# Performance work log

Measured on AMD Instinct MI355X. Metric: run time of the kernel, lower is better.

Reference implementation:

```python
import jax, jax.numpy as jnp
import numpy as np

B, S, D = 2, 2048, 2048
HQ, HKV, HD, HDV = 32, 8, 64, 64
QPK = HQ // HKV
EPS = 1e-5


def setup_inputs() -> dict:
    key = jax.random.key(0)
    ks = jax.random.split(key, 10)
    s = lambda fan_in: 1.0 / np.sqrt(fan_in)
    return {
        'x': jax.random.normal(ks[0], (B, S, D), dtype=jnp.float32),
        'ln_g': jnp.ones((D,), jnp.float32),
        'ln_b': jnp.zeros((D,), jnp.float32),
        'Wq': jax.random.uniform(ks[1], (D, HQ * HD), jnp.float32, -s(D), s(D)),
        'bq': jax.random.uniform(ks[2], (HQ * HD,), jnp.float32, -s(D), s(D)),
        'Wk': jax.random.uniform(ks[3], (D, HKV * HD), jnp.float32, -s(D), s(D)),
        'bk': jax.random.uniform(ks[4], (HKV * HD,), jnp.float32, -s(D), s(D)),
        'Wv': jax.random.uniform(ks[5], (D, HKV * HDV), jnp.float32, -s(D), s(D)),
        'bv': jax.random.uniform(ks[6], (HKV * HDV,), jnp.float32, -s(D), s(D)),
        'Wo': jax.random.uniform(ks[7], (HQ * HDV, D), jnp.float32, -s(HQ * HDV), s(HQ * HDV)),
        'bo': jax.random.uniform(ks[8], (D,), jnp.float32, -s(HQ * HDV), s(HQ * HDV)),
    }


def reference(x, ln_g, ln_b, Wq, bq, Wk, bk, Wv, bv, Wo, bo):
    # LayerNorm
    mu = jnp.mean(x, axis=-1, keepdims=True)
    var = jnp.mean(jnp.square(x - mu), axis=-1, keepdims=True)
    xn = (x - mu) * jax.lax.rsqrt(var + EPS) * ln_g + ln_b

    q = (xn @ Wq + bq).reshape(B, S, HKV, QPK, HD) * (1.0 / np.sqrt(HD))
    k = (xn @ Wk + bk).reshape(B, S, HKV, HD)
    v = (xn @ Wv + bv).reshape(B, S, HKV, HDV)

    # scores: (b, t=query, T=key, h, q_per_kv)
    scores = jnp.einsum('bthqd,bThd->btThq', q, k)
    # causal mask: -inf where T > t (upper triangle above diagonal)
    mask = jnp.triu(jnp.full((S, S), -jnp.inf, dtype=scores.dtype), 1)
    scores = scores + mask[None, :, :, None, None]
    # NOTE: source softmaxes over dim=-4, i.e. the QUERY axis t -> axis=1 here
    scores = jax.nn.softmax(scores, axis=1)
    out = jnp.einsum('btThq,bThd->bthqd', scores, v)
    out = out.reshape(B, S, HQ * HDV)
    return out @ Wo + bo
```

## Files before the change

### kernel.cpp

```cpp
#include <hip/hip_runtime.h>

#define Bb  2
#define Ss  2048
#define Dd  2048
#define HKV 8
#define QPK 4
#define HD  64
#define MR  (Bb * Ss)
#define NQ  2048
#define NKV 512

#define LOG2E 1.4426950408889634f

typedef unsigned short u16;
typedef unsigned int u32;
typedef __attribute__((ext_vector_type(8))) short s16x8;
typedef __attribute__((ext_vector_type(4))) float f32x4;

__device__ __forceinline__ u16 f2bf(float f) {
  unsigned u = __float_as_uint(f);
  u += 0x7fffu + ((u >> 16) & 1u);
  return (u16)(u >> 16);
}

__device__ __forceinline__ void gload16(const u16* g, u16* l) {
  __builtin_amdgcn_global_load_lds(
      (const __attribute__((address_space(1))) unsigned int*)g,
      (__attribute__((address_space(3))) unsigned int*)l, 16, 0, 0);
}

__device__ __forceinline__ u32 cvtpk_bf16(float a, float b) {
  u32 r;
  asm volatile("v_cvt_pk_bf16_f32 %0, %1, %2" : "=v"(r) : "v"(a), "v"(b));
  return r;
}

#define BAR()    asm volatile("s_barrier" ::: "memory")
#define WAITV4() asm volatile("s_waitcnt vmcnt(4)" ::: "memory")
#define WAITV0() asm volatile("s_waitcnt vmcnt(0)" ::: "memory")

__global__ __launch_bounds__(256) void ln_kernel(
    const float* __restrict__ x, const float* __restrict__ g,
    const float* __restrict__ be, u16* __restrict__ xn)
{
  int row = blockIdx.x;
  int tid = threadIdx.x;
  const float4* xr = (const float4*)(x + (size_t)row * Dd);
  float4 a = xr[tid];
  float4 b4 = xr[tid + 256];
  float s  = a.x + a.y + a.z + a.w + b4.x + b4.y + b4.z + b4.w;
  float ss = a.x*a.x + a.y*a.y + a.z*a.z + a.w*a.w
           + b4.x*b4.x + b4.y*b4.y + b4.z*b4.z + b4.w*b4.w;
  #pragma unroll
  for (int off = 32; off > 0; off >>= 1) {
    s  += __shfl_down(s, off);
    ss += __shfl_down(ss, off);
  }
  __shared__ float red[8];
  int lane = tid & 63, w = tid >> 6;
  if (lane == 0) { red[w] = s; red[4 + w] = ss; }
  __syncthreads();
  s  = red[0] + red[1] + red[2] + red[3];
  ss = red[4] + red[5] + red[6] + red[7];
  float mu = s * (1.0f / Dd);
  float rs = rsqrtf(ss * (1.0f / Dd) - mu * mu + 1e-5f);

  u16* xo = xn + (size_t)row * Dd;
  const float4* gv4 = (const float4*)g;
  const float4* bv4 = (const float4*)be;
  #pragma unroll
  for (int p = 0; p < 2; ++p) {
    int idx = tid + p * 256;
    float4 xv = (p == 0) ? a : b4;
    float4 gg = gv4[idx], bb = bv4[idx];
    ushort4 pk;
    pk.x = f2bf((xv.x - mu) * rs * gg.x + bb.x);
    pk.y = f2bf((xv.y - mu) * rs * gg.y + bb.y);
    pk.z = f2bf((xv.z - mu) * rs * gg.z + bb.z);
    pk.w = f2bf((xv.w - mu) * rs * gg.w + bb.w);
    *(ushort4*)(xo + idx * 4) = pk;
  }
}

__global__ __launch_bounds__(256) void transpose_cast(
    const float* __restrict__ W, u16* __restrict__ WT, int K, int N)
{
  __shared__ float tile[32][33];
  int tx = threadIdx.x & 31, ty = threadIdx.x >> 5;
  int n0 = blockIdx.x * 32, k0 = blockIdx.y * 32;
  #pragma unroll
  for (int i = 0; i < 4; ++i)
    tile[ty + 8 * i][tx] = W[(size_t)(k0 + ty + 8 * i) * N + n0 + tx];
  __syncthreads();
  #pragma unroll
  for (int i = 0; i < 4; ++i)
    WT[(size_t)(n0 + ty + 8 * i) * K + k0 + tx] = f2bf(tile[tx][ty + 8 * i]);
}

__global__ __launch_bounds__(256) void transpose_v(
    const u16* __restrict__ vb, u16* __restrict__ vT)
{
  __shared__ u16 tile[32][33];
  int tx = threadIdx.x & 31, ty = threadIdx.x >> 5;
  int c0 = blockIdx.x * 32;
  int r0 = blockIdx.y * 32;
  #pragma unroll
  for (int i = 0; i < 4; ++i)
    tile[ty + 8 * i][tx] = vb[(size_t)(r0 + ty + 8 * i) * NKV + c0 + tx];
  __syncthreads();
  int b = r0 >> 11, t = r0 & 2047;
  #pragma unroll
  for (int i = 0; i < 4; ++i)
    vT[((size_t)(b * NKV + c0 + ty + 8 * i)) * Ss + t + tx] = tile[tx][ty + 8 * i];
}

__device__ __forceinline__ void gemm8_core(
    const u16* __restrict__ A, const u16* __restrict__ BT, int K,
    int brow, int bcol, u16* __restrict__ As, u16* __restrict__ Bs,
    f32x4 (&acc)[8][4])
{
  const int tid  = threadIdx.x;
  const int lane = tid & 63;
  const int wave = tid >> 6;
  const int wr = wave >> 2, wc = wave & 3;
  const int m16 = lane & 15, quad = lane >> 4;
  const int NT = K >> 6;

  const int r0 = tid >> 3;
  const int sg = (tid & 7) ^ (r0 & 7);
  const u16* Asrc = A  + (size_t)(brow + r0) * K + sg * 8;
  const u16* Bsrc = BT + (size_t)(bcol + r0) * K + sg * 8;
  u16* AsW = As + wave * 512;
  u16* BsW = Bs + wave * 512;
  const size_t a64 = (size_t)64 * K;

  const int sl0 = (quad ^ (m16 & 7)) * 8;
  const int sl1 = ((quad | 4) ^ (m16 & 7)) * 8;
  const u16* Afr = As + wr * 8192 + m16 * 64;
  const u16* Bfr = Bs + (wc >> 1) * 8192 + ((wc & 1) * 64 + m16) * 64;

  #pragma unroll
  for (int h = 0; h < 2; ++h) {
    gload16(Asrc + (size_t)(h * 128) * K, AsW + h * 8192);
    gload16(Asrc + (size_t)(h * 128) * K + a64, AsW + h * 8192 + 4096);
    gload16(Bsrc + (size_t)(h * 128) * K, BsW + h * 8192);
    gload16(Bsrc + (size_t)(h * 128) * K + a64, BsW + h * 8192 + 4096);
  }
  #pragma unroll
  for (int h = 0; h < 2; ++h) {
    gload16(Bsrc + (size_t)(h * 128) * K + 64, BsW + 16384 + h * 8192);
    gload16(Bsrc + (size_t)(h * 128) * K + a64 + 64, BsW + 16384 + h * 8192 + 4096);
  }
  WAITV4();
  BAR();

  for (int t = 0; t < NT; ++t) {
    const int bi = t & 1;
    const u16* Abuf = Afr + bi * 16384;
    const u16* Bbuf = Bfr + bi * 16384;
    s16x8 bfr[4][2];
    #pragma unroll
    for (int ph = 0; ph < 4; ++ph) {
      s16x8 a0k0 = *(const s16x8*)(Abuf + (ph * 2 + 0) * 1024 + sl0);
      s16x8 a0k1 = *(const s16x8*)(Abuf + (ph * 2 + 0) * 1024 + sl1);
      s16x8 a1k0 = *(const s16x8*)(Abuf + (ph * 2 + 1) * 1024 + sl0);
      s16x8 a1k1 = *(const s16x8*)(Abuf + (ph * 2 + 1) * 1024 + sl1);
      if (ph == 0) {
        #pragma unroll
        for (int nj = 0; nj < 4; ++nj) {
          bfr[nj][0] = *(const s16x8*)(Bbuf + nj * 1024 + sl0);
          bfr[nj][1] = *(const s16x8*)(Bbuf + nj * 1024 + sl1);
        }
      }
      if (ph < 2) {
        if (t + 1 < NT) {
          const u16* g = Asrc + (size_t)(ph * 128) * K + (t + 1) * 64;
          u16* l = AsW + (bi ^ 1) * 16384 + ph * 8192;
          gload16(g, l);
          gload16(g + a64, l + 4096);
        }
      } else {
        if (t + 2 < NT) {
          const u16* g = Bsrc + (size_t)((ph - 2) * 128) * K + (t + 2) * 64;
          u16* l = BsW + bi * 16384 + (ph - 2) * 8192;
          gload16(g, l);
          gload16(g + a64, l + 4096);
        }
      }
      BAR();
      __builtin_amdgcn_s_setprio(1);
      #pragma unroll
      for (int nj = 0; nj < 4; ++nj) {
        acc[ph*2+0][nj] = __builtin_amdgcn_mfma_f32_16x16x32_bf16(a0k0, bfr[nj][0], acc[ph*2+0][nj], 0, 0, 0);
        acc[ph*2+0][nj] = __builtin_amdgcn_mfma_f32_16x16x32_bf16(a0k1, bfr[nj][1], acc[ph*2+0][nj], 0, 0, 0);
        acc[ph*2+1][nj] = __builtin_amdgcn_mfma_f32_16x16x32_bf16(a1k0, bfr[nj][0], acc[ph*2+1][nj], 0, 0, 0);
        acc[ph*2+1][nj] = __builtin_amdgcn_mfma_f32_16x16x32_bf16(a1k1, bfr[nj][1], acc[ph*2+1][nj], 0, 0, 0);
      }
      __builtin_amdgcn_s_setprio(0);
      if (ph == 3) {
        if (t + 2 < NT) WAITV4(); else WAITV0();
      }
      BAR();
    }
  }
}

__global__ __launch_bounds__(512) void gemm8_bt(
    const u16* __restrict__ A, const u16* __restrict__ BT,
    const float* __restrict__ bias, float* __restrict__ C, int N, int K)
{
  __shared__ u16 As[32768];
  __shared__ u16 Bs[32768];
  int nbx = N >> 8;
  int id  = blockIdx.y * nbx + blockIdx.x;
  int nwg = gridDim.x * gridDim.y;
  int swz = (id & 7) * (nwg >> 3) + (id >> 3);
  int bx = swz % nbx, by = swz / nbx;

  f32x4 acc[8][4] = {};
  gemm8_core(A, BT, K, by * 256, bx * 256, As, Bs, acc);

  int lane = threadIdx.x & 63, wave = threadIdx.x >> 6;
  int wr = wave >> 2, wc = wave & 3;
  int m16 = lane & 15, quad = lane >> 4;
  int colb = bx * 256 + (wc >> 1) * 128 + (wc & 1) * 64;
  #pragma unroll
  for (int nj = 0; nj < 4; ++nj) {
    int col = colb + nj * 16 + m16;
    float bc = bias[col];
    #pragma unroll
    for (int mi = 0; mi < 8; ++mi)
      #pragma unroll
      for (int rr = 0; rr < 4; ++rr) {
        int row = by * 256 + wr * 128 + mi * 16 + quad * 4 + rr;
        C[(size_t)row * N + col] = acc[mi][nj][rr] + bc;
      }
  }
}

__global__ __launch_bounds__(512) void gemm8_qkv(
    const u16* __restrict__ A, const u16* __restrict__ BT,
    const float* __restrict__ bq, const float* __restrict__ bk,
    const float* __restrict__ bv,
    u16* __restrict__ qb, u16* __restrict__ kb, u16* __restrict__ vb)
{
  __shared__ u16 As[32768];
  __shared__ u16 Bs[32768];
  int nbx = 12;
  int id  = blockIdx.y * nbx + blockIdx.x;
  int nwg = 192;
  int swz = (id & 7) * (nwg >> 3) + (id >> 3);
  int bx = swz % nbx, by = swz / nbx;

  f32x4 acc[8][4] = {};
  gemm8_core(A, BT, Dd, by * 256, bx * 256, As, Bs, acc);

  u16* outp; const float* bp; int ldo, cb; float scale;
  if (bx < 8)       { outp = qb; bp = bq; ldo = NQ;  cb = bx * 256;        scale = 0.125f * LOG2E; }
  else if (bx < 10) { outp = kb; bp = bk; ldo = NKV; cb = (bx - 8) * 256;  scale = 1.0f; }
  else              { outp = vb; bp = bv; ldo = NKV; cb = (bx - 10) * 256; scale = 1.0f; }

  int lane = threadIdx.x & 63, wave = threadIdx.x >> 6;
  int wr = wave >> 2, wc = wave & 3;
  int m16 = lane & 15, quad = lane >> 4;
  int colb = cb + (wc >> 1) * 128 + (wc & 1) * 64;
  #pragma unroll
  for (int nj = 0; nj < 4; ++nj) {
    int col = colb + nj * 16 + m16;
    float bc = bp[col];
    #pragma unroll
    for (int mi = 0; mi < 8; ++mi)
      #pragma unroll
      for (int rr = 0; rr < 4; ++rr) {
        int row = by * 256 + wr * 128 + mi * 16 + quad * 4 + rr;
        outp[(size_t)row * ldo + col] = f2bf((acc[mi][nj][rr] + bc) * scale);
      }
  }
}

__global__ __launch_bounds__(256) void pass_a_mfma(
    const u16* __restrict__ qb, const u16* __restrict__ kb,
    float* __restrict__ cst)
{
  __shared__ u16 Qs[64 * 64];
  int combo = blockIdx.x;
  int qk = combo & 3, bh = combo >> 2;
  int b = bh >> 3, h = bh & 7;
  int g = blockIdx.y;
  int tid = threadIdx.x;
  int lane = tid & 63, wave = tid >> 6;
  int m16 = lane & 15, quad = lane >> 4;
  int T0w = g * 128 + wave * 32;

  const u16* kbase = kb + (size_t)b * Ss * NKV + h * HD;
  const u16* qbase = qb + (size_t)b * Ss * NQ + (h * QPK + qk) * HD;

  s16x8 kf[2][2];
  #pragma unroll
  for (int jg = 0; jg < 2; ++jg)
    #pragma unroll
    for (int dc = 0; dc < 2; ++dc)
      kf[jg][dc] = *(const s16x8*)(kbase + (size_t)(T0w + jg * 16 + m16) * NKV + dc * 32 + quad * 8);

  float ms[2] = {-1e30f, -1e30f};
  float ls[2] = {0.f, 0.f};
  int srow  = (wave << 3) + (lane >> 3);
  int slot0 = (lane & 7) ^ (lane >> 3);
  u16* QsW = Qs + (size_t)(wave * 8) * 64;
  int sl0 = quad ^ (m16 & 7);
  int sl1 = (quad | 4) ^ (m16 & 7);
  int tDiag = T0w & ~63;

  for (int t0 = g * 128; t0 < Ss; t0 += 64) {
    __syncthreads();
    gload16(qbase + (size_t)(t0 + srow) * NQ + slot0 * 8, QsW);
    gload16(qbase + (size_t)(t0 + srow + 32) * NQ + slot0 * 8, QsW + 32 * 64);
    __syncthreads();
    if (t0 + 63 < T0w) continue;

    s16x8 af[4][2];
    #pragma unroll
    for (int i = 0; i < 4; ++i) {
      af[i][0] = *(const s16x8*)&Qs[(i * 16 + m16) * 64 + sl0 * 8];
      af[i][1] = *(const s16x8*)&Qs[(i * 16 + m16) * 64 + sl1 * 8];
    }
    f32x4 acc[4][2];
    #pragma unroll
    for (int i = 0; i < 4; ++i)
      #pragma unroll
      for (int jg = 0; jg < 2; ++jg) {
        f32x4 z = {};
        z = __builtin_amdgcn_mfma_f32_16x16x32_bf16(af[i][0], kf[jg][0], z, 0, 0, 0);
        acc[i][jg] = __builtin_amdgcn_mfma_f32_16x16x32_bf16(af[i][1], kf[jg][1], z, 0, 0, 0);
      }
    if (t0 == tDiag) {
      #pragma unroll
      for (int i = 0; i < 4; ++i)
        #pragma unroll
        for (int jg = 0; jg < 2; ++jg) {
          int tg = t0 + i * 16 + quad * 4;
          int Tg = T0w + jg * 16 + m16;
          #pragma unroll
          for (int r = 0; r < 4; ++r)
            if (tg + r < Tg) acc[i][jg][r] = -3e38f;
        }
    }
    #pragma unroll
    for (int jg = 0; jg < 2; ++jg) {
      float bm = -3e38f;
      #pragma unroll
      for (int i = 0; i < 4; ++i)
        #pragma unroll
        for (int r = 0; r < 4; ++r) bm = fmaxf(bm, acc[i][jg][r]);
      float mn = fmaxf(ms[jg], bm);
      float se = 0.f;
      #pragma unroll
      for (int i = 0; i < 4; ++i)
        #pragma unroll
        for (int r = 0; r < 4; ++r) se += exp2f(acc[i][jg][r] - mn);
      ls[jg] = ls[jg] * exp2f(ms[jg] - mn) + se;
      ms[jg] = mn;
    }
  }
  #pragma unroll
  for (int jg = 0; jg < 2; ++jg) {
    float m = ms[jg], l = ls[jg];
    #pragma unroll
    for (int off = 16; off <= 32; off <<= 1) {
      float mo = __shfl_xor(m, off);
      float lo = __shfl_xor(l, off);
      float mn = fmaxf(m, mo);
      l = l * exp2f(m - mn) + lo * exp2f(mo - mn);
      m = mn;
    }
    if (quad == 0)
      cst[(size_t)(bh * QPK + qk) * Ss + T0w + jg * 16 + m16] = m + __log2f(l);
  }
}

__global__ __launch_bounds__(256) void pass_b_mfma(
    const u16* __restrict__ qb, const u16* __restrict__ kb,
    const u16* __restrict__ vT, const float* __restrict__ cst,
    u16* __restrict__ attn)
{
  __shared__ u16 Ks[64 * 64];
  __shared__ u16 Vs[64 * 64];
  int combo = blockIdx.x;
  int qk = combo & 3, bh = combo >> 2;
  int b = bh >> 3, h = bh & 7;
  int g = 31 - blockIdx.y;
  int tid = threadIdx.x;
  int lane = tid & 63, wave = tid >> 6;
  int m16 = lane & 15, quad = lane >> 4;
  int trow = g * 64 + wave * 16;

  const u16* qbase = qb + (size_t)b * Ss * NQ + (h * QPK + qk) * HD;
  const u16* kbase = kb + (size_t)b * Ss * NKV + h * HD;
  const u16* vbase = vT + (size_t)(bh * 64) * Ss;
  const float* cbase = cst + (size_t)(bh * QPK + qk) * Ss;

  s16x8 qf[2];
  #pragma unroll
  for (int dc = 0; dc < 2; ++dc)
    qf[dc] = *(const s16x8*)(qbase + (size_t)(trow + m16) * NQ + dc * 32 + quad * 8);

  f32x4 oacc[4] = {};
  int srow  = (wave << 3) + (lane >> 3);
  int slot0 = (lane & 7) ^ (lane >> 3);
  u16* KsW = Ks + (size_t)(wave * 8) * 64;
  u16* VsW = Vs + (size_t)(wave * 8) * 64;
  int sl0 = quad ^ (m16 & 7);
  int sl1 = (quad | 4) ^ (m16 & 7);
  int Tend = g * 64;

  for (int T0 = 0; T0 <= Tend; T0 += 64) {
    __syncthreads();
    gload16(kbase + (size_t)(T0 + srow) * NKV + slot0 * 8, KsW);
    gload16(kbase + (size_t)(T0 + srow + 32) * NKV + slot0 * 8, KsW + 32 * 64);
    gload16(vbase + (size_t)srow * Ss + T0 + slot0 * 8, VsW);
    gload16(vbase + (size_t)(srow + 32) * Ss + T0 + slot0 * 8, VsW + 32 * 64);
    __syncthreads();
    bool diag = (T0 == Tend);
    #pragma unroll
    for (int tc = 0; tc < 2; ++tc) {
      u32 A[2], Bw[2];
      #pragma unroll
      for (int ii = 0; ii < 2; ++ii) {
        int i = tc * 2 + ii;
        s16x8 k0 = *(const s16x8*)&Ks[(i * 16 + m16) * 64 + sl0 * 8];
        s16x8 k1 = *(const s16x8*)&Ks[(i * 16 + m16) * 64 + sl1 * 8];
        f32x4 z = {};
        z = __builtin_amdgcn_mfma_f32_16x16x32_bf16(k0, qf[0], z, 0, 0, 0);
        z = __builtin_amdgcn_mfma_f32_16x16x32_bf16(k1, qf[1], z, 0, 0, 0);
        float4 cc = *(const float4*)(cbase + T0 + i * 16 + quad * 4);
        float w0 = exp2f(z[0] - cc.x);
        float w1 = exp2f(z[1] - cc.y);
        float w2 = exp2f(z[2] - cc.z);
        float w3 = exp2f(z[3] - cc.w);
        if (diag) {
          int t  = trow + m16;
          int Tg = T0 + i * 16 + quad * 4;
          if (Tg + 0 > t) w0 = 0.f;
          if (Tg + 1 > t) w1 = 0.f;
          if (Tg + 2 > t) w2 = 0.f;
          if (Tg + 3 > t) w3 = 0.f;
        }
        A[ii]  = cvtpk_bf16(w0, w1);
        Bw[ii] = cvtpk_bf16(w2, w3);
      }
      asm volatile("v_permlane32_swap_b32 %0, %1" : "+v"(A[0]),  "+v"(A[1]));
      asm volatile("v_permlane16_swap_b32 %0, %1" : "+v"(A[0]),  "+v"(A[1]));
      asm volatile("v_permlane32_swap_b32 %0, %1" : "+v"(Bw[0]), "+v"(Bw[1]));
      asm volatile("v_permlane16_swap_b32 %0, %1" : "+v"(Bw[0]), "+v"(Bw[1]));
      union { uint4 u; s16x8 v; } pu;
      pu.u.x = A[0]; pu.u.y = Bw[0]; pu.u.z = A[1]; pu.u.w = Bw[1];
      s16x8 pa = pu.v;
      #pragma unroll
      for (int dj = 0; dj < 4; ++dj) {
        int vsl = (quad | (tc << 2)) ^ (m16 & 7);
        s16x8 vf = *(const s16x8*)&Vs[(dj * 16 + m16) * 64 + vsl * 8];
        oacc[dj] = __builtin_amdgcn_mfma_f32_16x16x32_bf16(pa, vf, oacc[dj], 0, 0, 0);
      }
    }
  }
  u16* abase = attn + (size_t)b * Ss * NQ + (h * QPK + qk) * HD;
  #pragma unroll
  for (int dj = 0; dj < 4; ++dj)
    #pragma unroll
    for (int r = 0; r < 4; ++r)
      abase[(size_t)(trow + quad * 4 + r) * NQ + dj * 16 + m16] = f2bf(oacc[dj][r]);
}

extern "C" void kernel_launch(void* const* d_in, const int* in_sizes, int n_in,
                              void* d_out, int out_size, void* d_ws, size_t ws_size,
                              hipStream_t stream)
{
  (void)in_sizes; (void)n_in; (void)out_size; (void)ws_size;
  const float* x   = (const float*)d_in[0];
  const float* lng = (const float*)d_in[1];
  const float* lnb = (const float*)d_in[2];
  const float* Wq  = (const float*)d_in[3];
  const float* bq  = (const float*)d_in[4];
  const float* Wk  = (const float*)d_in[5];
  const float* bk  = (const float*)d_in[6];
  const float* Wv  = (const float*)d_in[7];
  const float* bv  = (const float*)d_in[8];
  const float* Wo  = (const float*)d_in[9];
  const float* bo  = (const float*)d_in[10];
  float* out = (float*)d_out;

  char* ws = (char*)d_ws;
  size_t off = 0;
  auto take = [&](size_t bytes) -> char* {
    char* p = ws + off;
    off += (bytes + 255) & ~(size_t)255;
    return p;
  };
  u16*    xnb   = (u16*)take((size_t)MR * Dd * 2);
  u16*    wqkvT = (u16*)take((size_t)(NQ + 2 * NKV) * Dd * 2);
  u16*    woT   = (u16*)take((size_t)Dd * NQ * 2);
  u16*    qbB   = (u16*)take((size_t)MR * NQ * 2);
  u16*    kbB   = (u16*)take((size_t)MR * NKV * 2);
  u16*    vbB   = (u16*)take((size_t)MR * NKV * 2);
  u16*    vTb   = (u16*)take((size_t)MR * NKV * 2);
  float*  cst   = (float*)take((size_t)Bb * HKV * QPK * Ss * 4);
  u16*    attnb = (u16*)take((size_t)MR * NQ * 2);

  ln_kernel<<<MR, 256, 0, stream>>>(x, lng, lnb, xnb);
  transpose_cast<<<dim3(NQ / 32, Dd / 32), 256, 0, stream>>>(Wq, wqkvT, Dd, NQ);
  transpose_cast<<<dim3(NKV / 32, Dd / 32), 256, 0, stream>>>(Wk, wqkvT + (size_t)NQ * Dd, Dd, NKV);
  transpose_cast<<<dim3(NKV / 32, Dd / 32), 256, 0, stream>>>(Wv, wqkvT + (size_t)(NQ + NKV) * Dd, Dd, NKV);
  transpose_cast<<<dim3(NQ / 32, Dd / 32), 256, 0, stream>>>(Wo, woT, Dd, NQ);

  gemm8_qkv<<<dim3(12, 16), 512, 0, stream>>>(xnb, wqkvT, bq, bk, bv, qbB, kbB, vbB);
  transpose_v<<<dim3(NKV / 32, MR / 32), 256, 0, stream>>>(vbB, vTb);

  pass_a_mfma<<<dim3(64, 16), 256, 0, stream>>>(qbB, kbB, cst);
  pass_b_mfma<<<dim3(64, 32), 256, 0, stream>>>(qbB, kbB, vTb, cst, attnb);

  gemm8_bt<<<dim3(8, 16), 512, 0, stream>>>(attnb, woT, bo, out, Dd, NQ);
}
```

Measured before the change: 385.6 us.

## Pair causal tiles for balanced attention blocks and use narrower output GEMM tiles

```diff
diff --git a/kernel.cpp b/kernel.cpp
--- a/kernel.cpp
+++ b/kernel.cpp
@@ -37,6 +37,7 @@
 
 #define BAR()    asm volatile("s_barrier" ::: "memory")
 #define WAITV4() asm volatile("s_waitcnt vmcnt(4)" ::: "memory")
+#define WAITV2() asm volatile("s_waitcnt vmcnt(2)" ::: "memory")
 #define WAITV0() asm volatile("s_waitcnt vmcnt(0)" ::: "memory")
 
 __global__ __launch_bounds__(256) void ln_kernel(
@@ -205,39 +206,6 @@
   }
 }
 
-__global__ __launch_bounds__(512) void gemm8_bt(
-    const u16* __restrict__ A, const u16* __restrict__ BT,
-    const float* __restrict__ bias, float* __restrict__ C, int N, int K)
-{
-  __shared__ u16 As[32768];
-  __shared__ u16 Bs[32768];
-  int nbx = N >> 8;
-  int id  = blockIdx.y * nbx + blockIdx.x;
-  int nwg = gridDim.x * gridDim.y;
-  int swz = (id & 7) * (nwg >> 3) + (id >> 3);
-  int bx = swz % nbx, by = swz / nbx;
-
-  f32x4 acc[8][4] = {};
-  gemm8_core(A, BT, K, by * 256, bx * 256, As, Bs, acc);
-
-  int lane = threadIdx.x & 63, wave = threadIdx.x >> 6;
-  int wr = wave >> 2, wc = wave & 3;
-  int m16 = lane & 15, quad = lane >> 4;
-  int colb = bx * 256 + (wc >> 1) * 128 + (wc & 1) * 64;
-  #pragma unroll
-  for (int nj = 0; nj < 4; ++nj) {
-    int col = colb + nj * 16 + m16;
-    float bc = bias[col];
-    #pragma unroll
-    for (int mi = 0; mi < 8; ++mi)
-      #pragma unroll
-      for (int rr = 0; rr < 4; ++rr) {
-        int row = by * 256 + wr * 128 + mi * 16 + quad * 4 + rr;
-        C[(size_t)row * N + col] = acc[mi][nj][rr] + bc;
-      }
-  }
-}
-
 __global__ __launch_bounds__(512) void gemm8_qkv(
     const u16* __restrict__ A, const u16* __restrict__ BT,
     const float* __restrict__ bq, const float* __restrict__ bk,
@@ -278,6 +246,117 @@
   }
 }
 
+__global__ __launch_bounds__(512) void gemm8_wo(
+    const u16* __restrict__ A, const u16* __restrict__ BT,
+    const float* __restrict__ bias, float* __restrict__ C, int N, int K)
+{
+  __shared__ u16 As[32768];
+  __shared__ u16 Bs[16384];
+  int nbx = N >> 7;
+  int id  = blockIdx.y * nbx + blockIdx.x;
+  int nwg = gridDim.x * gridDim.y;
+  int swz = (id & 7) * (nwg >> 3) + (id >> 3);
+  int bx = swz % nbx, by = swz / nbx;
+
+  const int tid  = threadIdx.x;
+  const int lane = tid & 63;
+  const int wave = tid >> 6;
+  const int wr = wave >> 2, wc = wave & 3;
+  const int m16 = lane & 15, quad = lane >> 4;
+  const int NT = K >> 6;
+
+  const int r0 = tid >> 3;
+  const int sg = (tid & 7) ^ (r0 & 7);
+  const u16* Asrc = A  + (size_t)(by * 256 + r0) * K + sg * 8;
+  const u16* Bsrc = BT + (size_t)(bx * 128 + r0) * K + sg * 8;
+  u16* AsW = As + wave * 512;
+  u16* BsW = Bs + wave * 512;
+  const size_t a64 = (size_t)64 * K;
+
+  const int sl0 = (quad ^ (m16 & 7)) * 8;
+  const int sl1 = ((quad | 4) ^ (m16 & 7)) * 8;
+  const u16* Afr = As + wr * 8192 + m16 * 64;
+  const u16* Bfr = Bs + (wc * 32 + m16) * 64;
+
+  f32x4 acc[8][2] = {};
+
+  #pragma unroll
+  for (int h = 0; h < 2; ++h) {
+    gload16(Asrc + (size_t)(h * 128) * K, AsW + h * 8192);
+    gload16(Asrc + (size_t)(h * 128) * K + a64, AsW + h * 8192 + 4096);
+  }
+  gload16(Bsrc, BsW);
+  gload16(Bsrc + a64, BsW + 4096);
+  gload16(Bsrc + 64, BsW + 8192);
+  gload16(Bsrc + a64 + 64, BsW + 8192 + 4096);
+  WAITV2();
+  BAR();
+
+  for (int t = 0; t < NT; ++t) {
+    const int bi = t & 1;
+    const u16* Abuf = Afr + bi * 16384;
+    const u16* Bbuf = Bfr + bi * 8192;
+    s16x8 bfr[2][2];
+    #pragma unroll
+    for (int ph = 0; ph < 4; ++ph) {
+      s16x8 a0k0 = *(const s16x8*)(Abuf + (ph * 2 + 0) * 1024 + sl0);
+      s16x8 a0k1 = *(const s16x8*)(Abuf + (ph * 2 + 0) * 1024 + sl1);
+      s16x8 a1k0 = *(const s16x8*)(Abuf + (ph * 2 + 1) * 1024 + sl0);
+      s16x8 a1k1 = *(const s16x8*)(Abuf + (ph * 2 + 1) * 1024 + sl1);
+      if (ph == 0) {
+        #pragma unroll
+        for (int nj = 0; nj < 2; ++nj) {
+          bfr[nj][0] = *(const s16x8*)(Bbuf + nj * 1024 + sl0);
+          bfr[nj][1] = *(const s16x8*)(Bbuf + nj * 1024 + sl1);
+        }
+      }
+      if (ph < 2) {
+        if (t + 1 < NT) {
+          const u16* g = Asrc + (size_t)(ph * 128) * K + (t + 1) * 64;
+          u16* l = AsW + (bi ^ 1) * 16384 + ph * 8192;
+          gload16(g, l);
+          gload16(g + a64, l + 4096);
+        }
+      } else if (ph == 2) {
+        if (t + 2 < NT) {
+          const u16* g = Bsrc + (size_t)(t + 2) * 64;
+          u16* l = BsW + bi * 8192;
+          gload16(g, l);
+          gload16(g + a64, l + 4096);
+        }
+      }
+      BAR();
+      __builtin_amdgcn_s_setprio(1);
+      #pragma unroll
+      for (int nj = 0; nj < 2; ++nj) {
+        acc[ph*2+0][nj] = __builtin_amdgcn_mfma_f32_16x16x32_bf16(a0k0, bfr[nj][0], acc[ph*2+0][nj], 0, 0, 0);
+        acc[ph*2+0][nj] = __builtin_amdgcn_mfma_f32_16x16x32_bf16(a0k1, bfr[nj][1], acc[ph*2+0][nj], 0, 0, 0);
+        acc[ph*2+1][nj] = __builtin_amdgcn_mfma_f32_16x16x32_bf16(a1k0, bfr[nj][0], acc[ph*2+1][nj], 0, 0, 0);
+        acc[ph*2+1][nj] = __builtin_amdgcn_mfma_f32_16x16x32_bf16(a1k1, bfr[nj][1], acc[ph*2+1][nj], 0, 0, 0);
+      }
+      __builtin_amdgcn_s_setprio(0);
+      if (ph == 3) {
+        if (t + 2 < NT) WAITV2(); else WAITV0();
+      }
+      BAR();
+    }
+  }
+
+  int colb = bx * 128 + wc * 32;
+  #pragma unroll
+  for (int nj = 0; nj < 2; ++nj) {
+    int col = colb + nj * 16 + m16;
+    float bc = bias[col];
+    #pragma unroll
+    for (int mi = 0; mi < 8; ++mi)
+      #pragma unroll
+      for (int rr = 0; rr < 4; ++rr) {
+        int row = by * 256 + wr * 128 + mi * 16 + quad * 4 + rr;
+        C[(size_t)row * N + col] = acc[mi][nj][rr] + bc;
+      }
+  }
+}
+
 __global__ __launch_bounds__(256) void pass_a_mfma(
     const u16* __restrict__ qb, const u16* __restrict__ kb,
     float* __restrict__ cst)
@@ -286,37 +365,42 @@
   int combo = blockIdx.x;
   int qk = combo & 3, bh = combo >> 2;
   int b = bh >> 3, h = bh & 7;
-  int g = blockIdx.y;
+  int gi = blockIdx.y;
+  int gA = gi, gB = 15 - gi;
   int tid = threadIdx.x;
   int lane = tid & 63, wave = tid >> 6;
   int m16 = lane & 15, quad = lane >> 4;
-  int T0w = g * 128 + wave * 32;
+  int T0wA = gA * 128 + wave * 32;
+  int T0wB = gB * 128 + wave * 32;
 
   const u16* kbase = kb + (size_t)b * Ss * NKV + h * HD;
   const u16* qbase = qb + (size_t)b * Ss * NQ + (h * QPK + qk) * HD;
 
-  s16x8 kf[2][2];
+  s16x8 kfA[2][2], kfB[2][2];
   #pragma unroll
   for (int jg = 0; jg < 2; ++jg)
     #pragma unroll
-    for (int dc = 0; dc < 2; ++dc)
-      kf[jg][dc] = *(const s16x8*)(kbase + (size_t)(T0w + jg * 16 + m16) * NKV + dc * 32 + quad * 8);
-
-  float ms[2] = {-1e30f, -1e30f};
-  float ls[2] = {0.f, 0.f};
+    for (int dc = 0; dc < 2; ++dc) {
+      kfA[jg][dc] = *(const s16x8*)(kbase + (size_t)(T0wA + jg * 16 + m16) * NKV + dc * 32 + quad * 8);
+      kfB[jg][dc] = *(const s16x8*)(kbase + (size_t)(T0wB + jg * 16 + m16) * NKV + dc * 32 + quad * 8);
+    }
+
+  float msA[2] = {-1e30f, -1e30f}, lsA[2] = {0.f, 0.f};
+  float msB[2] = {-1e30f, -1e30f}, lsB[2] = {0.f, 0.f};
   int srow  = (wave << 3) + (lane >> 3);
   int slot0 = (lane & 7) ^ (lane >> 3);
   u16* QsW = Qs + (size_t)(wave * 8) * 64;
   int sl0 = quad ^ (m16 & 7);
   int sl1 = (quad | 4) ^ (m16 & 7);
-  int tDiag = T0w & ~63;
-
-  for (int t0 = g * 128; t0 < Ss; t0 += 64) {
+  int tDiagA = T0wA & ~63;
+  int tDiagB = T0wB & ~63;
+
+  for (int t0 = gA * 128; t0 < Ss; t0 += 64) {
     __syncthreads();
     gload16(qbase + (size_t)(t0 + srow) * NQ + slot0 * 8, QsW);
     gload16(qbase + (size_t)(t0 + srow + 32) * NQ + slot0 * 8, QsW + 32 * 64);
     __syncthreads();
-    if (t0 + 63 < T0w) continue;
+    if (t0 + 63 < T0wA) continue;
 
     s16x8 af[4][2];
     #pragma unroll
@@ -324,47 +408,88 @@
       af[i][0] = *(const s16x8*)&Qs[(i * 16 + m16) * 64 + sl0 * 8];
       af[i][1] = *(const s16x8*)&Qs[(i * 16 + m16) * 64 + sl1 * 8];
     }
-    f32x4 acc[4][2];
-    #pragma unroll
-    for (int i = 0; i < 4; ++i)
+    {
+      f32x4 acc[4][2];
+      #pragma unroll
+      for (int i = 0; i < 4; ++i)
+        #pragma unroll
+        for (int jg = 0; jg < 2; ++jg) {
+          f32x4 z = {};
+          z = __builtin_amdgcn_mfma_f32_16x16x32_bf16(af[i][0], kfA[jg][0], z, 0, 0, 0);
+          acc[i][jg] = __builtin_amdgcn_mfma_f32_16x16x32_bf16(af[i][1], kfA[jg][1], z, 0, 0, 0);
+        }
+      if (t0 == tDiagA) {
+        #pragma unroll
+        for (int i = 0; i < 4; ++i)
+          #pragma unroll
+          for (int jg = 0; jg < 2; ++jg) {
+            int tg = t0 + i * 16 + quad * 4;
+            int Tg = T0wA + jg * 16 + m16;
+            #pragma unroll
+            for (int r = 0; r < 4; ++r)
+              if (tg + r < Tg) acc[i][jg][r] = -3e38f;
+          }
+      }
       #pragma unroll
       for (int jg = 0; jg < 2; ++jg) {
-        f32x4 z = {};
-        z = __builtin_amdgcn_mfma_f32_16x16x32_bf16(af[i][0], kf[jg][0], z, 0, 0, 0);
-        acc[i][jg] = __builtin_amdgcn_mfma_f32_16x16x32_bf16(af[i][1], kf[jg][1], z, 0, 0, 0);
-      }
-    if (t0 == tDiag) {
+        float bm = -3e38f;
+        #pragma unroll
+        for (int i = 0; i < 4; ++i)
+          #pragma unroll
+          for (int r = 0; r < 4; ++r) bm = fmaxf(bm, acc[i][jg][r]);
+        float mn = fmaxf(msA[jg], bm);
+        float se = 0.f;
+        #pragma unroll
+        for (int i = 0; i < 4; ++i)
+          #pragma unroll
+          for (int r = 0; r < 4; ++r) se += exp2f(acc[i][jg][r] - mn);
+        lsA[jg] = lsA[jg] * exp2f(msA[jg] - mn) + se;
+        msA[jg] = mn;
+      }
+    }
+    if (t0 + 63 >= T0wB) {
+      f32x4 acc[4][2];
       #pragma unroll
       for (int i = 0; i < 4; ++i)
         #pragma unroll
         for (int jg = 0; jg < 2; ++jg) {
-          int tg = t0 + i * 16 + quad * 4;
-          int Tg = T0w + jg * 16 + m16;
+          f32x4 z = {};
+          z = __builtin_amdgcn_mfma_f32_16x16x32_bf16(af[i][0], kfB[jg][0], z, 0, 0, 0);
+          acc[i][jg] = __builtin_amdgcn_mfma_f32_16x16x32_bf16(af[i][1], kfB[jg][1], z, 0, 0, 0);
+        }
+      if (t0 == tDiagB) {
+        #pragma unroll
+        for (int i = 0; i < 4; ++i)
           #pragma unroll
-          for (int r = 0; r < 4; ++r)
-            if (tg + r < Tg) acc[i][jg][r] = -3e38f;
-        }
-    }
-    #pragma unroll
-    for (int jg = 0; jg < 2; ++jg) {
-      float bm = -3e38f;
-      #pragma unroll
-      for (int i = 0; i < 4; ++i)
-        #pragma unroll
-        for (int r = 0; r < 4; ++r) bm = fmaxf(bm, acc[i][jg][r]);
-      float mn = fmaxf(ms[jg], bm);
-      float se = 0.f;
-      #pragma unroll
-      for (int i = 0; i < 4; ++i)
-        #pragma unroll
-        for (int r = 0; r < 4; ++r) se += exp2f(acc[i][jg][r] - mn);
-      ls[jg] = ls[jg] * exp2f(ms[jg] - mn) + se;
-      ms[jg] = mn;
+          for (int jg = 0; jg < 2; ++jg) {
+            int tg = t0 + i * 16 + quad * 4;
+            int Tg = T0wB + jg * 16 + m16;
+            #pragma unroll
+            for (int r = 0; r < 4; ++r)
+              if (tg + r < Tg) acc[i][jg][r] = -3e38f;
+          }
+      }
+      #pragma unroll
+      for (int jg = 0; jg < 2; ++jg) {
+        float bm = -3e38f;
+        #pragma unroll
+        for (int i = 0; i < 4; ++i)
+          #pragma unroll
+          for (int r = 0; r < 4; ++r) bm = fmaxf(bm, acc[i][jg][r]);
+        float mn = fmaxf(msB[jg], bm);
+        float se = 0.f;
+        #pragma unroll
+        for (int i = 0; i < 4; ++i)
+          #pragma unroll
+          for (int r = 0; r < 4; ++r) se += exp2f(acc[i][jg][r] - mn);
+        lsB[jg] = lsB[jg] * exp2f(msB[jg] - mn) + se;
+        msB[jg] = mn;
+      }
     }
   }
   #pragma unroll
   for (int jg = 0; jg < 2; ++jg) {
-    float m = ms[jg], l = ls[jg];
+    float m = msA[jg], l = lsA[jg];
     #pragma unroll
     for (int off = 16; off <= 32; off <<= 1) {
       float mo = __shfl_xor(m, off);
@@ -374,7 +499,21 @@
       m = mn;
     }
     if (quad == 0)
-      cst[(size_t)(bh * QPK + qk) * Ss + T0w + jg * 16 + m16] = m + __log2f(l);
+      cst[(size_t)(bh * QPK + qk) * Ss + T0wA + jg * 16 + m16] = m + __log2f(l);
+  }
+  #pragma unroll
+  for (int jg = 0; jg < 2; ++jg) {
+    float m = msB[jg], l = lsB[jg];
+    #pragma unroll
+    for (int off = 16; off <= 32; off <<= 1) {
+      float mo = __shfl_xor(m, off);
+      float lo = __shfl_xor(l, off);
+      float mn = fmaxf(m, mo);
+      l = l * exp2f(m - mn) + lo * exp2f(mo - mn);
+      m = mn;
+    }
+    if (quad == 0)
+      cst[(size_t)(bh * QPK + qk) * Ss + T0wB + jg * 16 + m16] = m + __log2f(l);
   }
 }
 
@@ -388,78 +527,121 @@
   int combo = blockIdx.x;
   int qk = combo & 3, bh = combo >> 2;
   int b = bh >> 3, h = bh & 7;
-  int g = 31 - blockIdx.y;
+  int gi = blockIdx.y;
   int tid = threadIdx.x;
   int lane = tid & 63, wave = tid >> 6;
   int m16 = lane & 15, quad = lane >> 4;
-  int trow = g * 64 + wave * 16;
+  int trowH = (31 - gi) * 64 + wave * 16;
+  int trowL = gi * 64 + wave * 16;
+  int TendH = (31 - gi) * 64;
+  int TendL = gi * 64;
 
   const u16* qbase = qb + (size_t)b * Ss * NQ + (h * QPK + qk) * HD;
   const u16* kbase = kb + (size_t)b * Ss * NKV + h * HD;
   const u16* vbase = vT + (size_t)(bh * 64) * Ss;
   const float* cbase = cst + (size_t)(bh * QPK + qk) * Ss;
 
-  s16x8 qf[2];
-  #pragma unroll
-  for (int dc = 0; dc < 2; ++dc)
-    qf[dc] = *(const s16x8*)(qbase + (size_t)(trow + m16) * NQ + dc * 32 + quad * 8);
-
-  f32x4 oacc[4] = {};
+  s16x8 qfH[2], qfL[2];
+  #pragma unroll
+  for (int dc = 0; dc < 2; ++dc) {
+    qfH[dc] = *(const s16x8*)(qbase + (size_t)(trowH + m16) * NQ + dc * 32 + quad * 8);
+    qfL[dc] = *(const s16x8*)(qbase + (size_t)(trowL + m16) * NQ + dc * 32 + quad * 8);
+  }
+
+  f32x4 oaccH[4] = {}, oaccL[4] = {};
   int srow  = (wave << 3) + (lane >> 3);
   int slot0 = (lane & 7) ^ (lane >> 3);
   u16* KsW = Ks + (size_t)(wave * 8) * 64;
   u16* VsW = Vs + (size_t)(wave * 8) * 64;
   int sl0 = quad ^ (m16 & 7);
   int sl1 = (quad | 4) ^ (m16 & 7);
-  int Tend = g * 64;
-
-  for (int T0 = 0; T0 <= Tend; T0 += 64) {
+
+  for (int T0 = 0; T0 <= TendH; T0 += 64) {
     __syncthreads();
     gload16(kbase + (size_t)(T0 + srow) * NKV + slot0 * 8, KsW);
     gload16(kbase + (size_t)(T0 + srow + 32) * NKV + slot0 * 8, KsW + 32 * 64);
     gload16(vbase + (size_t)srow * Ss + T0 + slot0 * 8, VsW);
     gload16(vbase + (size_t)(srow + 32) * Ss + T0 + slot0 * 8, VsW + 32 * 64);
     __syncthreads();
-    bool diag = (T0 == Tend);
+    bool doL   = (T0 <= TendL);
+    bool diagH = (T0 == TendH);
+    bool diagL = (T0 == TendL);
     #pragma unroll
     for (int tc = 0; tc < 2; ++tc) {
-      u32 A[2], Bw[2];
+      u32 AH[2], BH[2], AL[2], BL[2];
       #pragma unroll
       for (int ii = 0; ii < 2; ++ii) {
         int i = tc * 2 + ii;
         s16x8 k0 = *(const s16x8*)&Ks[(i * 16 + m16) * 64 + sl0 * 8];
         s16x8 k1 = *(const s16x8*)&Ks[(i * 16 + m16) * 64 + sl1 * 8];
-        f32x4 z = {};
-        z = __builtin_amdgcn_mfma_f32_16x16x32_bf16(k0, qf[0], z, 0, 0, 0);
-        z = __builtin_amdgcn_mfma_f32_16x16x32_bf16(k1, qf[1], z, 0, 0, 0);
         float4 cc = *(const float4*)(cbase + T0 + i * 16 + quad * 4);
-        float w0 = exp2f(z[0] - cc.x);
-        float w1 = exp2f(z[1] - cc.y);
-        float w2 = exp2f(z[2] - cc.z);
-        float w3 = exp2f(z[3] - cc.w);
-        if (diag) {
-          int t  = trow + m16;
-          int Tg = T0 + i * 16 + quad * 4;
-          if (Tg + 0 > t) w0 = 0.f;
-          if (Tg + 1 > t) w1 = 0.f;
-          if (Tg + 2 > t) w2 = 0.f;
-          if (Tg + 3 > t) w3 = 0.f;
-        }
-        A[ii]  = cvtpk_bf16(w0, w1);
-        Bw[ii] = cvtpk_bf16(w2, w3);
-      }
-      asm volatile("v_permlane32_swap_b32 %0, %1" : "+v"(A[0]),  "+v"(A[1]));
-      asm volatile("v_permlane16_swap_b32 %0, %1" : "+v"(A[0]),  "+v"(A[1]));
-      asm volatile("v_permlane32_swap_b32 %0, %1" : "+v"(Bw[0]), "+v"(Bw[1]));
-      asm volatile("v_permlane16_swap_b32 %0, %1" : "+v"(Bw[0]), "+v"(Bw[1]));
-      union { uint4 u; s16x8 v; } pu;
-      pu.u.x = A[0]; pu.u.y = Bw[0]; pu.u.z = A[1]; pu.u.w = Bw[1];
-      s16x8 pa = pu.v;
-      #pragma unroll
-      for (int dj = 0; dj < 4; ++dj) {
-        int vsl = (quad | (tc << 2)) ^ (m16 & 7);
-        s16x8 vf = *(const s16x8*)&Vs[(dj * 16 + m16) * 64 + vsl * 8];
-        oacc[dj] = __builtin_amdgcn_mfma_f32_16x16x32_bf16(pa, vf, oacc[dj], 0, 0, 0);
+        int Tg = T0 + i * 16 + quad * 4;
+        {
+          f32x4 z = {};
+          z = __builtin_amdgcn_mfma_f32_16x16x32_bf16(k0, qfH[0], z, 0, 0, 0);
+          z = __builtin_amdgcn_mfma_f32_16x16x32_bf16(k1, qfH[1], z, 0, 0, 0);
+          float w0 = exp2f(z[0] - cc.x);
+          float w1 = exp2f(z[1] - cc.y);
+          float w2 = exp2f(z[2] - cc.z);
+          float w3 = exp2f(z[3] - cc.w);
+          if (diagH) {
+            int t = trowH + m16;
+            if (Tg + 0 > t) w0 = 0.f;
+            if (Tg + 1 > t) w1 = 0.f;
+            if (Tg + 2 > t) w2 = 0.f;
+            if (Tg + 3 > t) w3 = 0.f;
+          }
+          AH[ii] = cvtpk_bf16(w0, w1);
+          BH[ii] = cvtpk_bf16(w2, w3);
+        }
+        if (doL) {
+          f32x4 z = {};
+          z = __builtin_amdgcn_mfma_f32_16x16x32_bf16(k0, qfL[0], z, 0, 0, 0);
+          z = __builtin_amdgcn_mfma_f32_16x16x32_bf16(k1, qfL[1], z, 0, 0, 0);
+          float w0 = exp2f(z[0] - cc.x);
+          float w1 = exp2f(z[1] - cc.y);
+          float w2 = exp2f(z[2] - cc.z);
+          float w3 = exp2f(z[3] - cc.w);
+          if (diagL) {
+            int t = trowL + m16;
+            if (Tg + 0 > t) w0 = 0.f;
+            if (Tg + 1 > t) w1 = 0.f;
+            if (Tg + 2 > t) w2 = 0.f;
+            if (Tg + 3 > t) w3 = 0.f;
+          }
+          AL[ii] = cvtpk_bf16(w0, w1);
+          BL[ii] = cvtpk_bf16(w2, w3);
+        }
+      }
+      asm volatile("v_permlane32_swap_b32 %0, %1" : "+v"(AH[0]), "+v"(AH[1]));
+      asm volatile("v_permlane16_swap_b32 %0, %1" : "+v"(AH[0]), "+v"(AH[1]));
+      asm volatile("v_permlane32_swap_b32 %0, %1" : "+v"(BH[0]), "+v"(BH[1]));
+      asm volatile("v_permlane16_swap_b32 %0, %1" : "+v"(BH[0]), "+v"(BH[1]));
+      {
+        union { uint4 u; s16x8 v; } pu;
+        pu.u.x = AH[0]; pu.u.y = BH[0]; pu.u.z = AH[1]; pu.u.w = BH[1];
+        s16x8 pa = pu.v;
+        #pragma unroll
+        for (int dj = 0; dj < 4; ++dj) {
+          int vsl = (quad | (tc << 2)) ^ (m16 & 7);
+          s16x8 vf = *(const s16x8*)&Vs[(dj * 16 + m16) * 64 + vsl * 8];
+          oaccH[dj] = __builtin_amdgcn_mfma_f32_16x16x32_bf16(pa, vf, oaccH[dj], 0, 0, 0);
+        }
+      }
+      if (doL) {
+        asm volatile("v_permlane32_swap_b32 %0, %1" : "+v"(AL[0]), "+v"(AL[1]));
+        asm volatile("v_permlane16_swap_b32 %0, %1" : "+v"(AL[0]), "+v"(AL[1]));
+        asm volatile("v_permlane32_swap_b32 %0, %1" : "+v"(BL[0]), "+v"(BL[1]));
+        asm volatile("v_permlane16_swap_b32 %0, %1" : "+v"(BL[0]), "+v"(BL[1]));
+        union { uint4 u; s16x8 v; } pu;
+        pu.u.x = AL[0]; pu.u.y = BL[0]; pu.u.z = AL[1]; pu.u.w = BL[1];
+        s16x8 pa = pu.v;
+        #pragma unroll
+        for (int dj = 0; dj < 4; ++dj) {
+          int vsl = (quad | (tc << 2)) ^ (m16 & 7);
+          s16x8 vf = *(const s16x8*)&Vs[(dj * 16 + m16) * 64 + vsl * 8];
+          oaccL[dj] = __builtin_amdgcn_mfma_f32_16x16x32_bf16(pa, vf, oaccL[dj], 0, 0, 0);
+        }
       }
     }
   }
@@ -467,8 +649,10 @@
   #pragma unroll
   for (int dj = 0; dj < 4; ++dj)
     #pragma unroll
-    for (int r = 0; r < 4; ++r)
-      abase[(size_t)(trow + quad * 4 + r) * NQ + dj * 16 + m16] = f2bf(oacc[dj][r]);
+    for (int r = 0; r < 4; ++r) {
+      abase[(size_t)(trowH + quad * 4 + r) * NQ + dj * 16 + m16] = f2bf(oaccH[dj][r]);
+      abase[(size_t)(trowL + quad * 4 + r) * NQ + dj * 16 + m16] = f2bf(oaccL[dj][r]);
+    }
 }
 
 extern "C" void kernel_launch(void* const* d_in, const int* in_sizes, int n_in,
@@ -515,8 +699,8 @@
   gemm8_qkv<<<dim3(12, 16), 512, 0, stream>>>(xnb, wqkvT, bq, bk, bv, qbB, kbB, vbB);
   transpose_v<<<dim3(NKV / 32, MR / 32), 256, 0, stream>>>(vbB, vTb);
 
-  pass_a_mfma<<<dim3(64, 16), 256, 0, stream>>>(qbB, kbB, cst);
-  pass_b_mfma<<<dim3(64, 32), 256, 0, stream>>>(qbB, kbB, vTb, cst, attnb);
-
-  gemm8_bt<<<dim3(8, 16), 512, 0, stream>>>(attnb, woT, bo, out, Dd, NQ);
-}
+  pass_a_mfma<<<dim3(64, 8), 256, 0, stream>>>(qbB, kbB, cst);
+  pass_b_mfma<<<dim3(64, 16), 256, 0, stream>>>(qbB, kbB, vTb, cst, attnb);
+
+  gemm8_wo<<<dim3(16, 16), 512, 0, stream>>>(attnb, woT, bo, out, Dd, NQ);
+}
```

Result: slower. 430.1 us (+11.5%).

## Double-buffer Q/K tiles in attention passes and use 256x128 output GEMM tiles

Applied to the files above, without the earlier changes.

```diff
diff --git a/kernel.cpp b/kernel.cpp
--- a/kernel.cpp
+++ b/kernel.cpp
@@ -37,6 +37,7 @@
 
 #define BAR()    asm volatile("s_barrier" ::: "memory")
 #define WAITV4() asm volatile("s_waitcnt vmcnt(4)" ::: "memory")
+#define WAITV2() asm volatile("s_waitcnt vmcnt(2)" ::: "memory")
 #define WAITV0() asm volatile("s_waitcnt vmcnt(0)" ::: "memory")
 
 __global__ __launch_bounds__(256) void ln_kernel(
@@ -205,39 +206,6 @@
   }
 }
 
-__global__ __launch_bounds__(512) void gemm8_bt(
-    const u16* __restrict__ A, const u16* __restrict__ BT,
-    const float* __restrict__ bias, float* __restrict__ C, int N, int K)
-{
-  __shared__ u16 As[32768];
-  __shared__ u16 Bs[32768];
-  int nbx = N >> 8;
-  int id  = blockIdx.y * nbx + blockIdx.x;
-  int nwg = gridDim.x * gridDim.y;
-  int swz = (id & 7) * (nwg >> 3) + (id >> 3);
-  int bx = swz % nbx, by = swz / nbx;
-
-  f32x4 acc[8][4] = {};
-  gemm8_core(A, BT, K, by * 256, bx * 256, As, Bs, acc);
-
-  int lane = threadIdx.x & 63, wave = threadIdx.x >> 6;
-  int wr = wave >> 2, wc = wave & 3;
-  int m16 = lane & 15, quad = lane >> 4;
-  int colb = bx * 256 + (wc >> 1) * 128 + (wc & 1) * 64;
-  #pragma unroll
-  for (int nj = 0; nj < 4; ++nj) {
-    int col = colb + nj * 16 + m16;
-    float bc = bias[col];
-    #pragma unroll
-    for (int mi = 0; mi < 8; ++mi)
-      #pragma unroll
-      for (int rr = 0; rr < 4; ++rr) {
-        int row = by * 256 + wr * 128 + mi * 16 + quad * 4 + rr;
-        C[(size_t)row * N + col] = acc[mi][nj][rr] + bc;
-      }
-  }
-}
-
 __global__ __launch_bounds__(512) void gemm8_qkv(
     const u16* __restrict__ A, const u16* __restrict__ BT,
     const float* __restrict__ bq, const float* __restrict__ bk,
@@ -278,11 +246,122 @@
   }
 }
 
+__global__ __launch_bounds__(512) void gemm8_wo(
+    const u16* __restrict__ A, const u16* __restrict__ BT,
+    const float* __restrict__ bias, float* __restrict__ C, int N, int K)
+{
+  __shared__ u16 As[32768];
+  __shared__ u16 Bs[16384];
+  int nbx = N >> 7;
+  int id  = blockIdx.y * nbx + blockIdx.x;
+  int nwg = gridDim.x * gridDim.y;
+  int swz = (id & 7) * (nwg >> 3) + (id >> 3);
+  int bx = swz % nbx, by = swz / nbx;
+
+  const int tid  = threadIdx.x;
+  const int lane = tid & 63;
+  const int wave = tid >> 6;
+  const int wr = wave >> 2, wc = wave & 3;
+  const int m16 = lane & 15, quad = lane >> 4;
+  const int NT = K >> 6;
+
+  const int r0 = tid >> 3;
+  const int sg = (tid & 7) ^ (r0 & 7);
+  const u16* Asrc = A  + (size_t)(by * 256 + r0) * K + sg * 8;
+  const u16* Bsrc = BT + (size_t)(bx * 128 + r0) * K + sg * 8;
+  u16* AsW = As + wave * 512;
+  u16* BsW = Bs + wave * 512;
+  const size_t a64 = (size_t)64 * K;
+
+  const int sl0 = (quad ^ (m16 & 7)) * 8;
+  const int sl1 = ((quad | 4) ^ (m16 & 7)) * 8;
+  const u16* Afr = As + wr * 8192 + m16 * 64;
+  const u16* Bfr = Bs + (wc * 32 + m16) * 64;
+
+  f32x4 acc[8][2] = {};
+
+  #pragma unroll
+  for (int h = 0; h < 2; ++h) {
+    gload16(Asrc + (size_t)(h * 128) * K, AsW + h * 8192);
+    gload16(Asrc + (size_t)(h * 128) * K + a64, AsW + h * 8192 + 4096);
+  }
+  gload16(Bsrc, BsW);
+  gload16(Bsrc + a64, BsW + 4096);
+  gload16(Bsrc + 64, BsW + 8192);
+  gload16(Bsrc + a64 + 64, BsW + 8192 + 4096);
+  WAITV2();
+  BAR();
+
+  for (int t = 0; t < NT; ++t) {
+    const int bi = t & 1;
+    const u16* Abuf = Afr + bi * 16384;
+    const u16* Bbuf = Bfr + bi * 8192;
+    s16x8 bfr[2][2];
+    #pragma unroll
+    for (int ph = 0; ph < 4; ++ph) {
+      s16x8 a0k0 = *(const s16x8*)(Abuf + (ph * 2 + 0) * 1024 + sl0);
+      s16x8 a0k1 = *(const s16x8*)(Abuf + (ph * 2 + 0) * 1024 + sl1);
+      s16x8 a1k0 = *(const s16x8*)(Abuf + (ph * 2 + 1) * 1024 + sl0);
+      s16x8 a1k1 = *(const s16x8*)(Abuf + (ph * 2 + 1) * 1024 + sl1);
+      if (ph == 0) {
+        #pragma unroll
+        for (int nj = 0; nj < 2; ++nj) {
+          bfr[nj][0] = *(const s16x8*)(Bbuf + nj * 1024 + sl0);
+          bfr[nj][1] = *(const s16x8*)(Bbuf + nj * 1024 + sl1);
+        }
+      }
+      if (ph < 2) {
+        if (t + 1 < NT) {
+          const u16* g = Asrc + (size_t)(ph * 128) * K + (t + 1) * 64;
+          u16* l = AsW + (bi ^ 1) * 16384 + ph * 8192;
+          gload16(g, l);
+          gload16(g + a64, l + 4096);
+        }
+      } else if (ph == 2) {
+        if (t + 2 < NT) {
+          const u16* g = Bsrc + (size_t)(t + 2) * 64;
+          u16* l = BsW + bi * 8192;
+          gload16(g, l);
+          gload16(g + a64, l + 4096);
+        }
+      }
+      BAR();
+      __builtin_amdgcn_s_setprio(1);
+      #pragma unroll
+      for (int nj = 0; nj < 2; ++nj) {
+        acc[ph*2+0][nj] = __builtin_amdgcn_mfma_f32_16x16x32_bf16(a0k0, bfr[nj][0], acc[ph*2+0][nj], 0, 0, 0);
+        acc[ph*2+0][nj] = __builtin_amdgcn_mfma_f32_16x16x32_bf16(a0k1, bfr[nj][1], acc[ph*2+0][nj], 0, 0, 0);
+        acc[ph*2+1][nj] = __builtin_amdgcn_mfma_f32_16x16x32_bf16(a1k0, bfr[nj][0], acc[ph*2+1][nj], 0, 0, 0);
+        acc[ph*2+1][nj] = __builtin_amdgcn_mfma_f32_16x16x32_bf16(a1k1, bfr[nj][1], acc[ph*2+1][nj], 0, 0, 0);
+      }
+      __builtin_amdgcn_s_setprio(0);
+      if (ph == 3) {
+        if (t + 2 < NT) WAITV2(); else WAITV0();
+      }
+      BAR();
+    }
+  }
+
+  int colb = bx * 128 + wc * 32;
+  #pragma unroll
+  for (int nj = 0; nj < 2; ++nj) {
+    int col = colb + nj * 16 + m16;
+    float bc = bias[col];
+    #pragma unroll
+    for (int mi = 0; mi < 8; ++mi)
+      #pragma unroll
+      for (int rr = 0; rr < 4; ++rr) {
+        int row = by * 256 + wr * 128 + mi * 16 + quad * 4 + rr;
+        C[(size_t)row * N + col] = acc[mi][nj][rr] + bc;
+      }
+  }
+}
+
 __global__ __launch_bounds__(256) void pass_a_mfma(
     const u16* __restrict__ qb, const u16* __restrict__ kb,
     float* __restrict__ cst)
 {
-  __shared__ u16 Qs[64 * 64];
+  __shared__ u16 Qs[2][64 * 64];
   int combo = blockIdx.x;
   int qk = combo & 3, bh = combo >> 2;
   int b = bh >> 3, h = bh & 7;
@@ -306,23 +385,37 @@
   float ls[2] = {0.f, 0.f};
   int srow  = (wave << 3) + (lane >> 3);
   int slot0 = (lane & 7) ^ (lane >> 3);
-  u16* QsW = Qs + (size_t)(wave * 8) * 64;
   int sl0 = quad ^ (m16 & 7);
   int sl1 = (quad | 4) ^ (m16 & 7);
   int tDiag = T0w & ~63;
 
-  for (int t0 = g * 128; t0 < Ss; t0 += 64) {
-    __syncthreads();
+  {
+    u16* QsW = &Qs[0][(wave * 8) * 64];
+    int t0 = g * 128;
     gload16(qbase + (size_t)(t0 + srow) * NQ + slot0 * 8, QsW);
     gload16(qbase + (size_t)(t0 + srow + 32) * NQ + slot0 * 8, QsW + 32 * 64);
-    __syncthreads();
-    if (t0 + 63 < T0w) continue;
-
+  }
+
+  for (int t0 = g * 128; t0 < Ss; t0 += 64) {
+    int cur = (t0 >> 6) & 1;
+    bool nxt = (t0 + 64 < Ss);
+    if (nxt) {
+      u16* QsW = &Qs[cur ^ 1][(wave * 8) * 64];
+      gload16(qbase + (size_t)(t0 + 64 + srow) * NQ + slot0 * 8, QsW);
+      gload16(qbase + (size_t)(t0 + 64 + srow + 32) * NQ + slot0 * 8, QsW + 32 * 64);
+      WAITV2();
+    } else {
+      WAITV0();
+    }
+    BAR();
+    if (t0 + 63 < T0w) { BAR(); continue; }
+
+    const u16* Qc = &Qs[cur][0];
     s16x8 af[4][2];
     #pragma unroll
     for (int i = 0; i < 4; ++i) {
-      af[i][0] = *(const s16x8*)&Qs[(i * 16 + m16) * 64 + sl0 * 8];
-      af[i][1] = *(const s16x8*)&Qs[(i * 16 + m16) * 64 + sl1 * 8];
+      af[i][0] = *(const s16x8*)(Qc + (i * 16 + m16) * 64 + sl0 * 8);
+      af[i][1] = *(const s16x8*)(Qc + (i * 16 + m16) * 64 + sl1 * 8);
     }
     f32x4 acc[4][2];
     #pragma unroll
@@ -361,6 +454,7 @@
       ls[jg] = ls[jg] * exp2f(ms[jg] - mn) + se;
       ms[jg] = mn;
     }
+    BAR();
   }
   #pragma unroll
   for (int jg = 0; jg < 2; ++jg) {
@@ -383,8 +477,7 @@
     const u16* __restrict__ vT, const float* __restrict__ cst,
     u16* __restrict__ attn)
 {
-  __shared__ u16 Ks[64 * 64];
-  __shared__ u16 Vs[64 * 64];
+  __shared__ u16 Ks[2][64 * 64];
   int combo = blockIdx.x;
   int qk = combo & 3, bh = combo >> 2;
   int b = bh >> 3, h = bh & 7;
@@ -407,28 +500,38 @@
   f32x4 oacc[4] = {};
   int srow  = (wave << 3) + (lane >> 3);
   int slot0 = (lane & 7) ^ (lane >> 3);
-  u16* KsW = Ks + (size_t)(wave * 8) * 64;
-  u16* VsW = Vs + (size_t)(wave * 8) * 64;
   int sl0 = quad ^ (m16 & 7);
   int sl1 = (quad | 4) ^ (m16 & 7);
   int Tend = g * 64;
 
+  {
+    u16* KsW = &Ks[0][(wave * 8) * 64];
+    gload16(kbase + (size_t)srow * NKV + slot0 * 8, KsW);
+    gload16(kbase + (size_t)(srow + 32) * NKV + slot0 * 8, KsW + 32 * 64);
+  }
+
   for (int T0 = 0; T0 <= Tend; T0 += 64) {
-    __syncthreads();
-    gload16(kbase + (size_t)(T0 + srow) * NKV + slot0 * 8, KsW);
-    gload16(kbase + (size_t)(T0 + srow + 32) * NKV + slot0 * 8, KsW + 32 * 64);
-    gload16(vbase + (size_t)srow * Ss + T0 + slot0 * 8, VsW);
-    gload16(vbase + (size_t)(srow + 32) * Ss + T0 + slot0 * 8, VsW + 32 * 64);
-    __syncthreads();
+    int cur = (T0 >> 6) & 1;
+    bool nxt = (T0 + 64 <= Tend);
+    if (nxt) {
+      u16* KsW = &Ks[cur ^ 1][(wave * 8) * 64];
+      gload16(kbase + (size_t)(T0 + 64 + srow) * NKV + slot0 * 8, KsW);
+      gload16(kbase + (size_t)(T0 + 64 + srow + 32) * NKV + slot0 * 8, KsW + 32 * 64);
+      WAITV2();
+    } else {
+      WAITV0();
+    }
+    BAR();
     bool diag = (T0 == Tend);
+    const u16* Kc = &Ks[cur][0];
     #pragma unroll
     for (int tc = 0; tc < 2; ++tc) {
       u32 A[2], Bw[2];
       #pragma unroll
       for (int ii = 0; ii < 2; ++ii) {
         int i = tc * 2 + ii;
-        s16x8 k0 = *(const s16x8*)&Ks[(i * 16 + m16) * 64 + sl0 * 8];
-        s16x8 k1 = *(const s16x8*)&Ks[(i * 16 + m16) * 64 + sl1 * 8];
+        s16x8 k0 = *(const s16x8*)(Kc + (i * 16 + m16) * 64 + sl0 * 8);
+        s16x8 k1 = *(const s16x8*)(Kc + (i * 16 + m16) * 64 + sl1 * 8);
         f32x4 z = {};
         z = __builtin_amdgcn_mfma_f32_16x16x32_bf16(k0, qf[0], z, 0, 0, 0);
         z = __builtin_amdgcn_mfma_f32_16x16x32_bf16(k1, qf[1], z, 0, 0, 0);
@@ -457,11 +560,11 @@
       s16x8 pa = pu.v;
       #pragma unroll
       for (int dj = 0; dj < 4; ++dj) {
-        int vsl = (quad | (tc << 2)) ^ (m16 & 7);
-        s16x8 vf = *(const s16x8*)&Vs[(dj * 16 + m16) * 64 + vsl * 8];
+        s16x8 vf = *(const s16x8*)(vbase + (size_t)(dj * 16 + m16) * Ss + T0 + tc * 32 + quad * 8);
         oacc[dj] = __builtin_amdgcn_mfma_f32_16x16x32_bf16(pa, vf, oacc[dj], 0, 0, 0);
       }
     }
+    BAR();
   }
   u16* abase = attn + (size_t)b * Ss * NQ + (h * QPK + qk) * HD;
   #pragma unroll
@@ -518,5 +621,5 @@
   pass_a_mfma<<<dim3(64, 16), 256, 0, stream>>>(qbB, kbB, cst);
   pass_b_mfma<<<dim3(64, 32), 256, 0, stream>>>(qbB, kbB, vTb, cst, attnb);
 
-  gemm8_bt<<<dim3(8, 16), 512, 0, stream>>>(attnb, woT, bo, out, Dd, NQ);
-}
+  gemm8_wo<<<dim3(16, 16), 512, 0, stream>>>(attnb, woT, bo, out, Dd, NQ);
+}
```

Result: slower. 475.2 us (+23.2%).
